# Kernel optimization log

Hardware: AMD Instinct MI355X
Metric: run time of the kernel (lower is better)

The kernel has to match this reference:

```python
import math
import jax, jax.numpy as jnp
import numpy as np

NUM_HEADS = 16
SIZE = 1024
HEAD = SIZE // NUM_HEADS
MAX_SEQ = 2048
B, L = 4, 1024


def setup_inputs() -> dict:
    key = jax.random.key(0)
    ks = jax.random.split(key, 12)
    s = 1.0 / math.sqrt(SIZE)
    return {
        "k": jax.random.normal(ks[0], (B, L, SIZE), jnp.float32),
        "v": jax.random.normal(ks[1], (B, L, SIZE), jnp.float32),
        "q": jax.random.normal(ks[2], (B, L, SIZE), jnp.float32),
        "mask": jnp.ones((B, 1, L), dtype=bool),
        "E": jax.random.normal(ks[3], (MAX_SEQ, HEAD), jnp.float32),
        "Wk": jax.random.normal(ks[4], (SIZE, SIZE), jnp.float32) * s,
        "bk": jnp.zeros((SIZE,), jnp.float32),
        "Wv": jax.random.normal(ks[5], (SIZE, SIZE), jnp.float32) * s,
        "bv": jnp.zeros((SIZE,), jnp.float32),
        "Wq": jax.random.normal(ks[6], (SIZE, SIZE), jnp.float32) * s,
        "bq": jnp.zeros((SIZE,), jnp.float32),
        "Wo": jax.random.normal(ks[7], (SIZE, SIZE), jnp.float32) * s,
        "bo": jnp.zeros((SIZE,), jnp.float32),
    }


def _attention(k, v, q, mask, E, Wk, bk, Wv, bv, Wq, bq, Wo, bo):
    b, lk, d = k.shape
    lq = q.shape[1]
    hd = E.shape[1]
    h = d // hd
    # project and split heads -> [b, h, len, hd]
    kh = (k @ Wk + bk).reshape(b, lk, h, hd).transpose(0, 2, 1, 3)
    vh = (v @ Wv + bv).reshape(b, lk, h, hd).transpose(0, 2, 1, 3)
    qh = (q @ Wq + bq).reshape(b, lq, h, hd).transpose(0, 2, 1, 3)

    scores = jnp.einsum("bhqd,bhkd->bhqk", qh, kh)  # [b,h,lq,lk]

    # relative position bias (Music-Transformer skewing)
    e = E[E.shape[0] - lq:, :]                       # [lq, hd]
    QE = jnp.einsum("bhld,md->bhlm", qh, e)          # [b,h,lq,lq]
    tri = (jnp.arange(lq)[None, :] <= jnp.arange(lq)[:, None]).astype(QE.dtype)
    QE = QE * tri                                    # qe masking
    padded = jnp.pad(QE, ((0, 0), (0, 0), (0, 0), (1, 0)))  # pad left of last dim
    Srel = padded.reshape(b, h, lq + 1, lq)[:, :, 1:, :]      # [b,h,lq,lq]
    if lk > lq:
        Srel = jnp.pad(Srel, ((0, 0), (0, 0), (0, 0), (0, lk - lq)))
    elif lk < lq:
        Srel = Srel[:, :, :, :lk]
    scores = scores + Srel

    scores = scores / math.sqrt(hd)
    scores = jnp.where(mask[:, None], scores, -jnp.inf)  # mask [b,1,lk] -> [b,1,1,lk]
    attn = jax.nn.softmax(scores, axis=-1)
    ctx = jnp.einsum("bhqk,bhkd->bhqd", attn, vh)
    ctx = ctx.transpose(0, 2, 1, 3).reshape(b, lq, h * hd)
    return ctx @ Wo + bo


def reference(k, v, q, mask, E, Wk, bk, Wv, bv, Wq, bq, Wo, bo):
    return _attention(k, v, q, mask, E, Wk, bk, Wv, bv, Wq, bq, Wo, bo)
```

## Files before the change

### kernel.cpp

```cpp
#include <hip/hip_runtime.h>
#include <stdint.h>

typedef unsigned short u16;
typedef __attribute__((ext_vector_type(8))) short short8;
typedef __attribute__((ext_vector_type(4))) float f32x4;
typedef __attribute__((ext_vector_type(4))) unsigned short u16x4;

#define MFMA16(a, b, c) __builtin_amdgcn_mfma_f32_16x16x32_bf16((a), (b), (c), 0, 0, 0)

__device__ __forceinline__ float bf2f(u16 u) {
    union { uint32_t i; float f; } v;
    v.i = ((uint32_t)u) << 16;
    return v.f;
}
__device__ __forceinline__ u16 f2bf(float f) {
    union { float f; uint32_t i; } v;
    v.f = f;
    uint32_t r = v.i + 0x7FFF + ((v.i >> 16) & 1);
    return (u16)(r >> 16);
}
__device__ __forceinline__ float scrub(float x) {
    union { float f; uint32_t i; } v;
    v.f = x;
    return ((v.i & 0x7F800000u) == 0x7F800000u) ? 0.f : x;
}

__global__ __launch_bounds__(256) void transpose4(
    const float* __restrict__ W0, const float* __restrict__ W1,
    const float* __restrict__ W2, const float* __restrict__ W3,
    u16* __restrict__ out)
{
    __shared__ u16 t[32][33];
    int z = blockIdx.z;
    const float* W = (z == 0) ? W0 : (z == 1) ? W1 : (z == 2) ? W2 : W3;
    u16* o = out + (size_t)z * 1048576;
    int tx = threadIdx.x & 31, ty = threadIdx.x >> 5;
    int x = blockIdx.x * 32 + tx;
    int yb = blockIdx.y * 32;
#pragma unroll
    for (int j = 0; j < 4; j++)
        t[ty + j * 8][tx] = f2bf(W[(size_t)(yb + ty + j * 8) * 1024 + x]);
    __syncthreads();
    int xo = yb + tx;
    int yob = blockIdx.x * 32;
#pragma unroll
    for (int j = 0; j < 4; j++)
        o[(size_t)(yob + ty + j * 8) * 1024 + xo] = t[tx][ty + j * 8];
}

__global__ __launch_bounds__(256) void ecvt(
    const float* __restrict__ e, u16* __restrict__ eb)
{
    int i = (blockIdx.x * 256 + threadIdx.x) * 4;
    f32x4 v = *(const f32x4*)&e[i];
    u16x4 o;
#pragma unroll
    for (int r = 0; r < 4; r++) o[r] = f2bf(v[r]);
    *(u16x4*)&eb[i] = o;
}

__global__ __launch_bounds__(256) void cvt3(
    const float* __restrict__ a0, const float* __restrict__ a1,
    const float* __restrict__ a2, u16* __restrict__ o0,
    u16* __restrict__ o1, u16* __restrict__ o2)
{
    int z = blockIdx.y;
    const float* a = (z == 0) ? a0 : (z == 1) ? a1 : a2;
    u16* o = (z == 0) ? o0 : (z == 1) ? o1 : o2;
    int i = (blockIdx.x * 256 + threadIdx.x) * 4;
    f32x4 v = *(const f32x4*)&a[i];
    u16x4 p;
#pragma unroll
    for (int r = 0; r < 4; r++) p[r] = f2bf(v[r]);
    *(u16x4*)&o[i] = p;
}

__global__ __launch_bounds__(256) void gemm_qkv(
    const u16* __restrict__ A0, const u16* __restrict__ A1,
    const u16* __restrict__ A2, const u16* __restrict__ Wt,
    const float* __restrict__ bi0, const float* __restrict__ bi1,
    const float* __restrict__ bi2, u16* __restrict__ khp,
    u16* __restrict__ vhtp, u16* __restrict__ qhp)
{
    __shared__ u16 As[128][40];
    __shared__ u16 Bs[128][40];
    const int K = 1024;
    int z = blockIdx.z;
    const u16* A = (z == 0) ? A0 : (z == 1) ? A1 : A2;
    const float* bias = (z == 0) ? bi0 : (z == 1) ? bi1 : bi2;
    const u16* Bt = Wt + (size_t)z * 1048576;
    u16* outb = (z == 0) ? khp : (z == 1) ? vhtp : qhp;

    int n0 = blockIdx.x * 128, m0 = blockIdx.y * 128;
    int tid = threadIdx.x;
    int w = tid >> 6, lane = tid & 63, g = lane >> 4, cc = lane & 15;
    int wm = (w >> 1) * 64, wn = (w & 1) * 64;
    int tr = tid >> 2, tc = (tid & 3) * 8;

    f32x4 acc[4][4];
#pragma unroll
    for (int i = 0; i < 4; i++)
#pragma unroll
        for (int j = 0; j < 4; j++) acc[i][j] = (f32x4){0.f, 0.f, 0.f, 0.f};

    for (int kb = 0; kb < K; kb += 32) {
        short8 a0 = *(const short8*)&A[(size_t)(m0 + tr) * K + kb + tc];
        short8 a1 = *(const short8*)&A[(size_t)(m0 + 64 + tr) * K + kb + tc];
        short8 b0 = *(const short8*)&Bt[(size_t)(n0 + tr) * K + kb + tc];
        short8 b1 = *(const short8*)&Bt[(size_t)(n0 + 64 + tr) * K + kb + tc];
        __syncthreads();
        *(short8*)&As[tr][tc] = a0;
        *(short8*)&As[64 + tr][tc] = a1;
        *(short8*)&Bs[tr][tc] = b0;
        *(short8*)&Bs[64 + tr][tc] = b1;
        __syncthreads();
        short8 af[4], bf[4];
#pragma unroll
        for (int mt = 0; mt < 4; mt++) af[mt] = *(const short8*)&As[wm + mt * 16 + cc][g * 8];
#pragma unroll
        for (int nt = 0; nt < 4; nt++) bf[nt] = *(const short8*)&Bs[wn + nt * 16 + cc][g * 8];
#pragma unroll
        for (int mt = 0; mt < 4; mt++)
#pragma unroll
            for (int nt = 0; nt < 4; nt++)
                acc[mt][nt] = MFMA16(af[mt], bf[nt], acc[mt][nt]);
    }

#pragma unroll
    for (int mt = 0; mt < 4; mt++) {
        int rl = wm + mt * 16 + g * 4;
#pragma unroll
        for (int nt = 0; nt < 4; nt++) {
            int n = n0 + wn + nt * 16 + cc;
            float bb = bias[n];
            if (z == 1) {
                int m = m0 + rl;
                int b_ = m >> 10, l_ = m & 1023, h_ = n >> 6, d_ = n & 63;
                u16x4 pk;
#pragma unroll
                for (int r = 0; r < 4; r++) pk[r] = f2bf(scrub(acc[mt][nt][r] + bb));
                *(u16x4*)&outb[((size_t)(b_ * 16 + h_) * 64 + d_) * 1024 + l_] = pk;
            } else {
#pragma unroll
                for (int r = 0; r < 4; r++) {
                    int m = m0 + rl + r;
                    int b_ = m >> 10, l_ = m & 1023, h_ = n >> 6, d_ = n & 63;
                    outb[((size_t)(b_ * 16 + h_) * 1024 + l_) * 64 + d_] =
                        f2bf(scrub(acc[mt][nt][r] + bb));
                }
            }
        }
    }
}

__global__ __launch_bounds__(256) void gemm_out(
    const u16* __restrict__ A, const u16* __restrict__ Bt,
    const float* __restrict__ bias, float* __restrict__ outf)
{
    __shared__ u16 As[64][40];
    __shared__ u16 Bs[128][40];
    const int K = 1024;
    int n0 = blockIdx.x * 128, m0 = blockIdx.y * 64;
    int tid = threadIdx.x;
    int w = tid >> 6, lane = tid & 63, g = lane >> 4, cc = lane & 15;
    int wm = (w >> 1) * 32, wn = (w & 1) * 64;
    int tr = tid >> 2, tc = (tid & 3) * 8;

    f32x4 acc[2][4];
#pragma unroll
    for (int i = 0; i < 2; i++)
#pragma unroll
        for (int j = 0; j < 4; j++) acc[i][j] = (f32x4){0.f, 0.f, 0.f, 0.f};

    for (int kb = 0; kb < K; kb += 32) {
        short8 a0 = *(const short8*)&A[(size_t)(m0 + tr) * K + kb + tc];
        short8 b0 = *(const short8*)&Bt[(size_t)(n0 + tr) * K + kb + tc];
        short8 b1 = *(const short8*)&Bt[(size_t)(n0 + 64 + tr) * K + kb + tc];
        __syncthreads();
        if (tr < 64) *(short8*)&As[tr][tc] = a0;
        *(short8*)&Bs[tr][tc] = b0;
        *(short8*)&Bs[64 + tr][tc] = b1;
        __syncthreads();
        short8 af[2], bf[4];
#pragma unroll
        for (int mt = 0; mt < 2; mt++) af[mt] = *(const short8*)&As[wm + mt * 16 + cc][g * 8];
#pragma unroll
        for (int nt = 0; nt < 4; nt++) bf[nt] = *(const short8*)&Bs[wn + nt * 16 + cc][g * 8];
#pragma unroll
        for (int mt = 0; mt < 2; mt++)
#pragma unroll
            for (int nt = 0; nt < 4; nt++)
                acc[mt][nt] = MFMA16(af[mt], bf[nt], acc[mt][nt]);
    }

#pragma unroll
    for (int mt = 0; mt < 2; mt++) {
        int rl = wm + mt * 16 + g * 4;
#pragma unroll
        for (int nt = 0; nt < 4; nt++) {
            int n = n0 + wn + nt * 16 + cc;
            float bb = bias[n];
#pragma unroll
            for (int r = 0; r < 4; r++)
                outf[(size_t)(m0 + rl + r) * 1024 + n] = scrub(acc[mt][nt][r] + bb);
        }
    }
}

__global__ __launch_bounds__(256) void qe_gemm(
    const u16* __restrict__ qh, const u16* __restrict__ eb, u16* __restrict__ QEm)
{
    __shared__ u16 As[128][40];
    __shared__ u16 Bs[128][40];
    int mb = blockIdx.x * 128;
    int qb = blockIdx.y * 128;
    int bh = blockIdx.z;
    const u16* A = qh + (size_t)bh * 65536;
    u16* O = QEm + (size_t)bh * 1048576;
    int tid = threadIdx.x;

    if (mb > qb + 127) {
        short8 zz = (short8){0, 0, 0, 0, 0, 0, 0, 0};
        int row8 = tid >> 4;
        int col8 = (tid & 15) * 8;
#pragma unroll
        for (int rr = 0; rr < 8; rr++)
            *(short8*)&O[(size_t)(qb + rr * 16 + row8) * 1024 + mb + col8] = zz;
        return;
    }

    int w = tid >> 6, lane = tid & 63, g = lane >> 4, cc = lane & 15;
    int wm = (w >> 1) * 64, wn = (w & 1) * 64;
    int tr = tid >> 2, tc = (tid & 3) * 8;

    f32x4 acc[4][4];
#pragma unroll
    for (int i = 0; i < 4; i++)
#pragma unroll
        for (int j = 0; j < 4; j++) acc[i][j] = (f32x4){0.f, 0.f, 0.f, 0.f};

#pragma unroll
    for (int kb = 0; kb < 64; kb += 32) {
        short8 a0 = *(const short8*)&A[(size_t)(qb + tr) * 64 + kb + tc];
        short8 a1 = *(const short8*)&A[(size_t)(qb + 64 + tr) * 64 + kb + tc];
        short8 b0 = *(const short8*)&eb[(size_t)(mb + tr) * 64 + kb + tc];
        short8 b1 = *(const short8*)&eb[(size_t)(mb + 64 + tr) * 64 + kb + tc];
        __syncthreads();
        *(short8*)&As[tr][tc] = a0;
        *(short8*)&As[64 + tr][tc] = a1;
        *(short8*)&Bs[tr][tc] = b0;
        *(short8*)&Bs[64 + tr][tc] = b1;
        __syncthreads();
        short8 af[4], bf[4];
#pragma unroll
        for (int mt = 0; mt < 4; mt++) af[mt] = *(const short8*)&As[wm + mt * 16 + cc][g * 8];
#pragma unroll
        for (int nt = 0; nt < 4; nt++) bf[nt] = *(const short8*)&Bs[wn + nt * 16 + cc][g * 8];
#pragma unroll
        for (int mt = 0; mt < 4; mt++)
#pragma unroll
            for (int nt = 0; nt < 4; nt++)
                acc[mt][nt] = MFMA16(af[mt], bf[nt], acc[mt][nt]);
    }

#pragma unroll
    for (int mt = 0; mt < 4; mt++)
#pragma unroll
        for (int nt = 0; nt < 4; nt++)
#pragma unroll
            for (int r = 0; r < 4; r++) {
                int qi = qb + wm + mt * 16 + g * 4 + r;
                int mm = mb + wn + nt * 16 + cc;
                u16 v = (mm <= qi) ? f2bf(scrub(acc[mt][nt][r])) : (u16)0;
                O[(size_t)qi * 1024 + mm] = v;
            }
}

__global__ __launch_bounds__(256) void flash(
    const u16* __restrict__ qh, const u16* __restrict__ kh,
    const u16* __restrict__ vht, const u16* __restrict__ QEm,
    u16* __restrict__ ctx)
{
    __shared__ u16 Plds[4][16][136];
    int qt = blockIdx.x, bh = blockIdx.y;
    int w = threadIdx.x >> 6, lane = threadIdx.x & 63, g = lane >> 4, cc = lane & 15;
    const u16* Q = qh + (size_t)bh * 65536;
    const u16* Kp = kh + (size_t)bh * 65536;
    const u16* Vp = vht + (size_t)bh * 65536;
    const u16* QE = QEm + (size_t)bh * 1048576;
    int q0 = qt * 64 + w * 16;

    short8 qf[2];
#pragma unroll
    for (int ks = 0; ks < 2; ks++)
        qf[ks] = *(const short8*)&Q[(size_t)(q0 + cc) * 64 + ks * 32 + g * 8];

    float mi[4], li[4];
    f32x4 O[4];
#pragma unroll
    for (int r = 0; r < 4; r++) { mi[r] = -1e30f; li[r] = 0.f; }
#pragma unroll
    for (int d = 0; d < 4; d++) O[d] = (f32x4){0.f, 0.f, 0.f, 0.f};

    const float LOG2E = 1.44269504088896f;

    for (int kt = 0; kt < 8; kt++) {
        int k0 = kt * 128;
        u16 cv[32];
#pragma unroll
        for (int r = 0; r < 4; r++) {
            int q = q0 + g * 4 + r;
#pragma unroll
            for (int nt = 0; nt < 8; nt++) {
                int k = k0 + nt * 16 + cc;
                bool lower = (k <= q);
                int row = lower ? q : (q + 1);
                int col = lower ? (1023 + k - q) : (k - q - 2);
                col = (col < 0) ? 0 : col;
                u16 v = QE[(size_t)row * 1024 + col];
                cv[nt * 4 + r] = (k == q + 1) ? (u16)0 : v;
            }
        }

        f32x4 sc[8];
#pragma unroll
        for (int nt = 0; nt < 8; nt++) sc[nt] = (f32x4){0.f, 0.f, 0.f, 0.f};
#pragma unroll
        for (int nt = 0; nt < 8; nt++) {
            short8 b0 = *(const short8*)&Kp[(size_t)(k0 + nt * 16 + cc) * 64 + g * 8];
            short8 b1 = *(const short8*)&Kp[(size_t)(k0 + nt * 16 + cc) * 64 + 32 + g * 8];
            sc[nt] = MFMA16(qf[0], b0, sc[nt]);
            sc[nt] = MFMA16(qf[1], b1, sc[nt]);
        }

#pragma unroll
        for (int nt = 0; nt < 8; nt++)
#pragma unroll
            for (int r = 0; r < 4; r++)
                sc[nt][r] = (sc[nt][r] + bf2f(cv[nt * 4 + r])) * 0.125f;

#pragma unroll
        for (int r = 0; r < 4; r++) {
            float mx = sc[0][r];
#pragma unroll
            for (int nt = 1; nt < 8; nt++) mx = fmaxf(mx, sc[nt][r]);
            mx = fmaxf(mx, __shfl_xor(mx, 1));
            mx = fmaxf(mx, __shfl_xor(mx, 2));
            mx = fmaxf(mx, __shfl_xor(mx, 4));
            mx = fmaxf(mx, __shfl_xor(mx, 8));
            float mnew = fmaxf(mi[r], mx);
            float alpha = exp2f((mi[r] - mnew) * LOG2E);
            mi[r] = mnew;
            float rs = 0.f;
#pragma unroll
            for (int nt = 0; nt < 8; nt++) {
                float p = exp2f((sc[nt][r] - mnew) * LOG2E);
                sc[nt][r] = p;
                rs += p;
            }
            rs += __shfl_xor(rs, 1);
            rs += __shfl_xor(rs, 2);
            rs += __shfl_xor(rs, 4);
            rs += __shfl_xor(rs, 8);
            li[r] = li[r] * alpha + rs;
#pragma unroll
            for (int d = 0; d < 4; d++) O[d][r] *= alpha;
        }

#pragma unroll
        for (int nt = 0; nt < 8; nt++)
#pragma unroll
            for (int r = 0; r < 4; r++)
                Plds[w][g * 4 + r][nt * 16 + cc] = f2bf(sc[nt][r]);

#pragma unroll
        for (int ks = 0; ks < 4; ks++) {
            short8 a = *(const short8*)&Plds[w][cc][ks * 32 + g * 8];
#pragma unroll
            for (int d = 0; d < 4; d++) {
                short8 vb = *(const short8*)&Vp[(size_t)(d * 16 + cc) * 1024 + k0 + ks * 32 + g * 8];
                O[d] = MFMA16(a, vb, O[d]);
            }
        }
    }

    int b_ = bh >> 4, h_ = bh & 15;
#pragma unroll
    for (int d = 0; d < 4; d++)
#pragma unroll
        for (int r = 0; r < 4; r++) {
            int l_ = q0 + g * 4 + r;
            ctx[((size_t)b_ * 1024 + l_) * 1024 + h_ * 64 + d * 16 + cc] =
                f2bf(O[d][r] / li[r]);
        }
}

extern "C" void kernel_launch(void* const* d_in, const int* in_sizes, int n_in,
                              void* d_out, int out_size, void* d_ws, size_t ws_size,
                              hipStream_t stream)
{
    const float *k_in = nullptr, *v_in = nullptr, *q_in = nullptr, *E = nullptr;
    const float* W[4] = {nullptr, nullptr, nullptr, nullptr};
    const float* bs[4] = {nullptr, nullptr, nullptr, nullptr};
    int nqkv = 0, nW = 0, nb = 0;
    for (int i = 0; i < n_in; i++) {
        int s = in_sizes[i];
        const float* p = (const float*)d_in[i];
        if (s == 4194304) {
            if (nqkv == 0) k_in = p; else if (nqkv == 1) v_in = p; else if (nqkv == 2) q_in = p;
            nqkv++;
        } else if (s == 131072) {
            E = p;
        } else if (s == 1048576) {
            if (nW < 4) W[nW] = p;
            nW++;
        } else if (s == 1024) {
            if (nb < 4) bs[nb] = p;
            nb++;
        }
    }

    char* ws = (char*)d_ws;
    u16* Wt   = (u16*)ws;
    u16* khp  = (u16*)(ws + (8u << 20));
    u16* vhtp = (u16*)(ws + (16u << 20));
    u16* qhp  = (u16*)(ws + (24u << 20));
    u16* ctxp = (u16*)(ws + (32u << 20));
    u16* eb   = (u16*)(ws + (40u << 20));
    u16* kb   = (u16*)(ws + (48u << 20));
    u16* vb   = (u16*)(ws + (56u << 20));
    u16* qb   = (u16*)(ws + (64u << 20));
    u16* QEm  = (u16*)(ws + (48u << 20));

    const size_t M1 = 1048576;
    transpose4<<<dim3(32, 32, 4), 256, 0, stream>>>(W[0], W[1], W[2], W[3], Wt);
    ecvt<<<dim3(64), 256, 0, stream>>>(E + 65536, eb);
    cvt3<<<dim3(4096, 3), 256, 0, stream>>>(k_in, v_in, q_in, kb, vb, qb);
    gemm_qkv<<<dim3(8, 32, 3), 256, 0, stream>>>(kb, vb, qb, Wt,
                                                 bs[0], bs[1], bs[2],
                                                 khp, vhtp, qhp);
    qe_gemm<<<dim3(8, 8, 64), 256, 0, stream>>>(qhp, eb, QEm);
    flash<<<dim3(16, 64), 256, 0, stream>>>(qhp, khp, vhtp, QEm, ctxp);
    gemm_out<<<dim3(8, 64), 256, 0, stream>>>(ctxp, Wt + 3 * M1, bs[3], (float*)d_out);
}
```

Before: 384.2 us.

## Stage skewed relative-bias rows through LDS and skip zero regions

The flash kernel now computes which tiles of the skewed Srel term can be nonzero and skips reading QE for the rest. Where it is needed, it loads one contiguous run of QE per query row into a per-wave LDS buffer with vector loads, replacing scattered per-element global gathers. The QE GEMM no longer writes zeros for upper-triangle blocks, since the new indexing never reads them. This cuts global traffic and uncoalesced loads, at the cost of more complex index arithmetic whose correctness depends on the range logic, plus extra LDS use.

```diff
diff --git a/kernel.cpp b/kernel.cpp
--- a/kernel.cpp
+++ b/kernel.cpp
@@ -3,6 +3,7 @@
 
 typedef unsigned short u16;
 typedef __attribute__((ext_vector_type(8))) short short8;
+typedef __attribute__((ext_vector_type(4))) short s16x4;
 typedef __attribute__((ext_vector_type(4))) float f32x4;
 typedef __attribute__((ext_vector_type(4))) unsigned short u16x4;
 
@@ -219,15 +220,7 @@
     u16* O = QEm + (size_t)bh * 1048576;
     int tid = threadIdx.x;
 
-    if (mb > qb + 127) {
-        short8 zz = (short8){0, 0, 0, 0, 0, 0, 0, 0};
-        int row8 = tid >> 4;
-        int col8 = (tid & 15) * 8;
-#pragma unroll
-        for (int rr = 0; rr < 8; rr++)
-            *(short8*)&O[(size_t)(qb + rr * 16 + row8) * 1024 + mb + col8] = zz;
-        return;
-    }
+    if (mb > qb + 127) return;
 
     int w = tid >> 6, lane = tid & 63, g = lane >> 4, cc = lane & 15;
     int wm = (w >> 1) * 64, wn = (w & 1) * 64;
@@ -282,12 +275,12 @@
     u16* __restrict__ ctx)
 {
     __shared__ u16 Plds[4][16][136];
+    __shared__ u16 QEl[4][16][140];
     int qt = blockIdx.x, bh = blockIdx.y;
     int w = threadIdx.x >> 6, lane = threadIdx.x & 63, g = lane >> 4, cc = lane & 15;
     const u16* Q = qh + (size_t)bh * 65536;
     const u16* Kp = kh + (size_t)bh * 65536;
     const u16* Vp = vht + (size_t)bh * 65536;
-    const u16* QE = QEm + (size_t)bh * 1048576;
     int q0 = qt * 64 + w * 16;
 
     short8 qf[2];
@@ -303,22 +296,31 @@
     for (int d = 0; d < 4; d++) O[d] = (f32x4){0.f, 0.f, 0.f, 0.f};
 
     const float LOG2E = 1.44269504088896f;
+    int srow = lane >> 2, c4 = lane & 3;
 
     for (int kt = 0; kt < 8; kt++) {
         int k0 = kt * 128;
-        u16 cv[32];
-#pragma unroll
-        for (int r = 0; r < 4; r++) {
-            int q = q0 + g * 4 + r;
-#pragma unroll
-            for (int nt = 0; nt < 8; nt++) {
-                int k = k0 + nt * 16 + cc;
-                bool lower = (k <= q);
-                int row = lower ? q : (q + 1);
-                int col = lower ? (1023 + k - q) : (k - q - 2);
-                col = (col < 0) ? 0 : col;
-                u16 v = QE[(size_t)row * 1024 + col];
-                cv[nt * 4 + r] = (k == q + 1) ? (u16)0 : v;
+        int qw1 = q0 + 15;
+        bool need = (k0 <= 2 * qw1 - 1023) ||
+                    ((k0 + 127 >= q0 + 2) && (k0 <= 2 * qw1 + 3));
+
+        short8 stg[5];
+        size_t g0 = 0;
+        if (need) {
+            int qs = q0 + srow;
+            size_t S = (size_t)qs * 1023 + 1022 + (size_t)k0;
+            size_t A = S & ~(size_t)7;
+            g0 = (size_t)bh * 1048576 + A;
+#pragma unroll
+            for (int j = 0; j < 4; j++) {
+                size_t gi = g0 + (size_t)(c4 + 4 * j) * 8;
+                if (gi > 67108856) gi = 67108856;
+                stg[j] = *(const short8*)&QEm[gi];
+            }
+            if (c4 == 0) {
+                size_t gi = g0 + 128;
+                if (gi > 67108856) gi = 67108856;
+                stg[4] = *(const short8*)&QEm[gi];
             }
         }
 
@@ -333,11 +335,45 @@
             sc[nt] = MFMA16(qf[1], b1, sc[nt]);
         }
 
-#pragma unroll
-        for (int nt = 0; nt < 8; nt++)
-#pragma unroll
-            for (int r = 0; r < 4; r++)
-                sc[nt][r] = (sc[nt][r] + bf2f(cv[nt * 4 + r])) * 0.125f;
+        if (need) {
+#pragma unroll
+            for (int j = 0; j < 4; j++) {
+                int c = c4 + 4 * j;
+                s16x4 lo4 = __builtin_shufflevector(stg[j], stg[j], 0, 1, 2, 3);
+                s16x4 hi4 = __builtin_shufflevector(stg[j], stg[j], 4, 5, 6, 7);
+                *(s16x4*)&QEl[w][srow][c * 8] = lo4;
+                *(s16x4*)&QEl[w][srow][c * 8 + 4] = hi4;
+            }
+            if (c4 == 0) {
+                s16x4 lo4 = __builtin_shufflevector(stg[4], stg[4], 0, 1, 2, 3);
+                s16x4 hi4 = __builtin_shufflevector(stg[4], stg[4], 4, 5, 6, 7);
+                *(s16x4*)&QEl[w][srow][128] = lo4;
+                *(s16x4*)&QEl[w][srow][132] = hi4;
+            }
+        }
+
+#pragma unroll
+        for (int r = 0; r < 4; r++) {
+            int q = q0 + g * 4 + r;
+            int qoff = q - k0;
+            int lowlim = 2 * q - 1023 - k0;
+            int uphi = 2 * q + 3 - k0;
+            int dd = (1022 + k0 - q) & 7;
+            const u16* Lrow = &QEl[w][g * 4 + r][0];
+#pragma unroll
+            for (int nt = 0; nt < 8; nt++) {
+                int t = nt * 16 + cc;
+                float add = 0.f;
+                if (need) {
+                    bool lo = (t <= lowlim);
+                    bool up = (t >= qoff + 2) && (t <= uphi);
+                    int idx = dd + t + (lo ? 1 : 0);
+                    u16 vv = Lrow[idx];
+                    add = (lo || up) ? bf2f(vv) : 0.f;
+                }
+                sc[nt][r] = (sc[nt][r] + add) * 0.125f;
+            }
+        }
 
 #pragma unroll
         for (int r = 0; r < 4; r++) {
```

New measurement: 374.3 us. 2.6% less time.

## Write skewed Srel directly in GEMM epilogue and load it coalesced in flash

Applied to the files above, without the earlier changes.

The QE GEMM epilogue now scatters each element straight to its skewed Srel position, so the flash kernel no longer has to gather relative-position values with per-element index arithmetic. Flash instead loads contiguous 16x128 Srel tiles with vector loads, stages them through LDS to match the MFMA layout, and skips the load for tiles known to be zero. A small kernel zeroes the superdiagonal, and s_setprio hints are placed around the MFMA sections. The risks are scattered uncoalesced stores in the GEMM epilogue and extra LDS traffic in flash.

```diff
diff --git a/kernel.cpp b/kernel.cpp
--- a/kernel.cpp
+++ b/kernel.cpp
@@ -57,6 +57,16 @@
 #pragma unroll
     for (int r = 0; r < 4; r++) o[r] = f2bf(v[r]);
     *(u16x4*)&eb[i] = o;
+}
+
+__global__ __launch_bounds__(256) void diagz(u16* __restrict__ Sp)
+{
+    u16* O = Sp + (size_t)blockIdx.x * 1048576;
+#pragma unroll
+    for (int i = 0; i < 4; i++) {
+        int q = threadIdx.x * 4 + i;
+        if (q < 1023) O[(size_t)q * 1024 + q + 1] = 0;
+    }
 }
 
 __global__ __launch_bounds__(256) void cvt3(
@@ -207,8 +217,8 @@
     }
 }
 
-__global__ __launch_bounds__(256) void qe_gemm(
-    const u16* __restrict__ qh, const u16* __restrict__ eb, u16* __restrict__ QEm)
+__global__ __launch_bounds__(256) void srel_gemm(
+    const u16* __restrict__ qh, const u16* __restrict__ eb, u16* __restrict__ Sp)
 {
     __shared__ u16 As[128][40];
     __shared__ u16 Bs[128][40];
@@ -216,22 +226,10 @@
     int qb = blockIdx.y * 128;
     int bh = blockIdx.z;
     const u16* A = qh + (size_t)bh * 65536;
-    u16* O = QEm + (size_t)bh * 1048576;
+    u16* O = Sp + (size_t)bh * 1048576;
     int tid = threadIdx.x;
-
-    if (mb > qb + 127) {
-        short8 zz = (short8){0, 0, 0, 0, 0, 0, 0, 0};
-        int row8 = tid >> 4;
-        int col8 = (tid & 15) * 8;
-#pragma unroll
-        for (int rr = 0; rr < 8; rr++)
-            *(short8*)&O[(size_t)(qb + rr * 16 + row8) * 1024 + mb + col8] = zz;
-        return;
-    }
-
     int w = tid >> 6, lane = tid & 63, g = lane >> 4, cc = lane & 15;
     int wm = (w >> 1) * 64, wn = (w & 1) * 64;
-    int tr = tid >> 2, tc = (tid & 3) * 8;
 
     f32x4 acc[4][4];
 #pragma unroll
@@ -239,28 +237,31 @@
 #pragma unroll
         for (int j = 0; j < 4; j++) acc[i][j] = (f32x4){0.f, 0.f, 0.f, 0.f};
 
-#pragma unroll
-    for (int kb = 0; kb < 64; kb += 32) {
-        short8 a0 = *(const short8*)&A[(size_t)(qb + tr) * 64 + kb + tc];
-        short8 a1 = *(const short8*)&A[(size_t)(qb + 64 + tr) * 64 + kb + tc];
-        short8 b0 = *(const short8*)&eb[(size_t)(mb + tr) * 64 + kb + tc];
-        short8 b1 = *(const short8*)&eb[(size_t)(mb + 64 + tr) * 64 + kb + tc];
-        __syncthreads();
-        *(short8*)&As[tr][tc] = a0;
-        *(short8*)&As[64 + tr][tc] = a1;
-        *(short8*)&Bs[tr][tc] = b0;
-        *(short8*)&Bs[64 + tr][tc] = b1;
-        __syncthreads();
-        short8 af[4], bf[4];
-#pragma unroll
-        for (int mt = 0; mt < 4; mt++) af[mt] = *(const short8*)&As[wm + mt * 16 + cc][g * 8];
-#pragma unroll
-        for (int nt = 0; nt < 4; nt++) bf[nt] = *(const short8*)&Bs[wn + nt * 16 + cc][g * 8];
-#pragma unroll
-        for (int mt = 0; mt < 4; mt++)
-#pragma unroll
-            for (int nt = 0; nt < 4; nt++)
-                acc[mt][nt] = MFMA16(af[mt], bf[nt], acc[mt][nt]);
+    if (mb <= qb + 127) {
+        int tr = tid >> 2, tc = (tid & 3) * 8;
+#pragma unroll
+        for (int kb = 0; kb < 64; kb += 32) {
+            short8 a0 = *(const short8*)&A[(size_t)(qb + tr) * 64 + kb + tc];
+            short8 a1 = *(const short8*)&A[(size_t)(qb + 64 + tr) * 64 + kb + tc];
+            short8 b0 = *(const short8*)&eb[(size_t)(mb + tr) * 64 + kb + tc];
+            short8 b1 = *(const short8*)&eb[(size_t)(mb + 64 + tr) * 64 + kb + tc];
+            __syncthreads();
+            *(short8*)&As[tr][tc] = a0;
+            *(short8*)&As[64 + tr][tc] = a1;
+            *(short8*)&Bs[tr][tc] = b0;
+            *(short8*)&Bs[64 + tr][tc] = b1;
+            __syncthreads();
+            short8 af[4], bf[4];
+#pragma unroll
+            for (int mt = 0; mt < 4; mt++) af[mt] = *(const short8*)&As[wm + mt * 16 + cc][g * 8];
+#pragma unroll
+            for (int nt = 0; nt < 4; nt++) bf[nt] = *(const short8*)&Bs[wn + nt * 16 + cc][g * 8];
+#pragma unroll
+            for (int mt = 0; mt < 4; mt++)
+#pragma unroll
+                for (int nt = 0; nt < 4; nt++)
+                    acc[mt][nt] = MFMA16(af[mt], bf[nt], acc[mt][nt]);
+        }
     }
 
 #pragma unroll
@@ -269,25 +270,29 @@
         for (int nt = 0; nt < 4; nt++)
 #pragma unroll
             for (int r = 0; r < 4; r++) {
-                int qi = qb + wm + mt * 16 + g * 4 + r;
-                int mm = mb + wn + nt * 16 + cc;
-                u16 v = (mm <= qi) ? f2bf(scrub(acc[mt][nt][r])) : (u16)0;
-                O[(size_t)qi * 1024 + mm] = v;
+                int j = qb + wm + mt * 16 + g * 4 + r;
+                int c = mb + wn + nt * 16 + cc;
+                u16 v = (c <= j) ? f2bf(scrub(acc[mt][nt][r])) : (u16)0;
+                if (c >= 1023 - j)
+                    O[(size_t)j * 1024 + (c + j - 1023)] = v;
+                else if (j > 0)
+                    O[(size_t)(j - 1) * 1024 + (c + j + 1)] = v;
             }
 }
 
 __global__ __launch_bounds__(256) void flash(
     const u16* __restrict__ qh, const u16* __restrict__ kh,
-    const u16* __restrict__ vht, const u16* __restrict__ QEm,
+    const u16* __restrict__ vht, const u16* __restrict__ Sp,
     u16* __restrict__ ctx)
 {
     __shared__ u16 Plds[4][16][136];
+    __shared__ u16 SB[4][16][136];
     int qt = blockIdx.x, bh = blockIdx.y;
     int w = threadIdx.x >> 6, lane = threadIdx.x & 63, g = lane >> 4, cc = lane & 15;
     const u16* Q = qh + (size_t)bh * 65536;
     const u16* Kp = kh + (size_t)bh * 65536;
     const u16* Vp = vht + (size_t)bh * 65536;
-    const u16* QE = QEm + (size_t)bh * 1048576;
+    const u16* Sb = Sp + (size_t)bh * 1048576;
     int q0 = qt * 64 + w * 16;
 
     short8 qf[2];
@@ -303,28 +308,26 @@
     for (int d = 0; d < 4; d++) O[d] = (f32x4){0.f, 0.f, 0.f, 0.f};
 
     const float LOG2E = 1.44269504088896f;
+    int row = g * 4;
+    int srow = lane >> 2, c4 = lane & 3;
 
     for (int kt = 0; kt < 8; kt++) {
         int k0 = kt * 128;
-        u16 cv[32];
-#pragma unroll
-        for (int r = 0; r < 4; r++) {
-            int q = q0 + g * 4 + r;
-#pragma unroll
-            for (int nt = 0; nt < 8; nt++) {
-                int k = k0 + nt * 16 + cc;
-                bool lower = (k <= q);
-                int row = lower ? q : (q + 1);
-                int col = lower ? (1023 + k - q) : (k - q - 2);
-                col = (col < 0) ? 0 : col;
-                u16 v = QE[(size_t)row * 1024 + col];
-                cv[nt * 4 + r] = (k == q + 1) ? (u16)0 : v;
-            }
+        int qw1 = q0 + 15;
+        bool need = (k0 <= 2 * qw1 - 1023) ||
+                    ((k0 + 127 >= q0 + 2) && (k0 <= 2 * qw1 + 3));
+
+        short8 stg[4];
+        if (need) {
+            const u16* bp = &Sb[(size_t)(q0 + srow) * 1024 + k0 + c4 * 32];
+#pragma unroll
+            for (int j = 0; j < 4; j++) stg[j] = *(const short8*)&bp[j * 8];
         }
 
         f32x4 sc[8];
 #pragma unroll
         for (int nt = 0; nt < 8; nt++) sc[nt] = (f32x4){0.f, 0.f, 0.f, 0.f};
+        __builtin_amdgcn_s_setprio(1);
 #pragma unroll
         for (int nt = 0; nt < 8; nt++) {
             short8 b0 = *(const short8*)&Kp[(size_t)(k0 + nt * 16 + cc) * 64 + g * 8];
@@ -332,12 +335,25 @@
             sc[nt] = MFMA16(qf[0], b0, sc[nt]);
             sc[nt] = MFMA16(qf[1], b1, sc[nt]);
         }
+        __builtin_amdgcn_s_setprio(0);
+
+        if (need) {
+#pragma unroll
+            for (int j = 0; j < 4; j++)
+                *(short8*)&SB[w][srow][c4 * 32 + j * 8] = stg[j];
+#pragma unroll
+            for (int r = 0; r < 4; r++) {
+                const u16* Lr = &SB[w][row + r][0];
+#pragma unroll
+                for (int nt = 0; nt < 8; nt++)
+                    sc[nt][r] += bf2f(Lr[nt * 16 + cc]);
+            }
+        }
 
 #pragma unroll
         for (int nt = 0; nt < 8; nt++)
 #pragma unroll
-            for (int r = 0; r < 4; r++)
-                sc[nt][r] = (sc[nt][r] + bf2f(cv[nt * 4 + r])) * 0.125f;
+            for (int r = 0; r < 4; r++) sc[nt][r] *= 0.125f;
 
 #pragma unroll
         for (int r = 0; r < 4; r++) {
@@ -371,8 +387,9 @@
         for (int nt = 0; nt < 8; nt++)
 #pragma unroll
             for (int r = 0; r < 4; r++)
-                Plds[w][g * 4 + r][nt * 16 + cc] = f2bf(sc[nt][r]);
-
+                Plds[w][row + r][nt * 16 + cc] = f2bf(sc[nt][r]);
+
+        __builtin_amdgcn_s_setprio(1);
 #pragma unroll
         for (int ks = 0; ks < 4; ks++) {
             short8 a = *(const short8*)&Plds[w][cc][ks * 32 + g * 8];
@@ -382,6 +399,7 @@
                 O[d] = MFMA16(a, vb, O[d]);
             }
         }
+        __builtin_amdgcn_s_setprio(0);
     }
 
     int b_ = bh >> 4, h_ = bh & 15;
@@ -389,7 +407,7 @@
     for (int d = 0; d < 4; d++)
 #pragma unroll
         for (int r = 0; r < 4; r++) {
-            int l_ = q0 + g * 4 + r;
+            int l_ = q0 + row + r;
             ctx[((size_t)b_ * 1024 + l_) * 1024 + h_ * 64 + d * 16 + cc] =
                 f2bf(O[d][r] / li[r]);
         }
@@ -430,7 +448,7 @@
     u16* kb   = (u16*)(ws + (48u << 20));
     u16* vb   = (u16*)(ws + (56u << 20));
     u16* qb   = (u16*)(ws + (64u << 20));
-    u16* QEm  = (u16*)(ws + (48u << 20));
+    u16* Sp   = (u16*)(ws + (48u << 20));
 
     const size_t M1 = 1048576;
     transpose4<<<dim3(32, 32, 4), 256, 0, stream>>>(W[0], W[1], W[2], W[3], Wt);
@@ -439,7 +457,8 @@
     gemm_qkv<<<dim3(8, 32, 3), 256, 0, stream>>>(kb, vb, qb, Wt,
                                                  bs[0], bs[1], bs[2],
                                                  khp, vhtp, qhp);
-    qe_gemm<<<dim3(8, 8, 64), 256, 0, stream>>>(qhp, eb, QEm);
-    flash<<<dim3(16, 64), 256, 0, stream>>>(qhp, khp, vhtp, QEm, ctxp);
+    diagz<<<dim3(64), 256, 0, stream>>>(Sp);
+    srel_gemm<<<dim3(8, 8, 64), 256, 0, stream>>>(qhp, eb, Sp);
+    flash<<<dim3(16, 64), 256, 0, stream>>>(qhp, khp, vhtp, Sp, ctxp);
     gemm_out<<<dim3(8, 64), 256, 0, stream>>>(ctxp, Wt + 3 * M1, bs[3], (float*)d_out);
 }
```

After: 442.1 us. 1.15x slower.
